# Performance work log

Hardware: AMD Instinct MI355X
Metric: run time of the kernel (lower is better)

The kernel has to match this reference:

```python
import jax, jax.numpy as jnp
import numpy as np

DIM = 512
HEADS = 8
HEAD_DIM = DIM // HEADS
SCALE = HEAD_DIM ** -0.5
CPB_HIDDEN = 512
N_CLASSES = 2
LN_EPS = 1e-5


def _layernorm(x, g, b):
    m = jnp.mean(x, axis=-1, keepdims=True)
    v = jnp.var(x, axis=-1, keepdims=True)
    return (x - m) / jnp.sqrt(v + LN_EPS) * g + b


def _coord_attention(x, coords, cpb_w1, cpb_b1, cpb_w2, cpb_b2, qkv_w, qkv_b, proj_w, proj_b):
    B, N, C = x.shape
    qkv = (x @ qkv_w + qkv_b).reshape(B, N, 3, HEADS, HEAD_DIM)
    q, k, v = jnp.moveaxis(qkv, 2, 0)  # each (B, N, H, hd)
    attn = jnp.einsum('bnhd,bmhd->bhnm', q * SCALE, k)  # (B, H, N, N)
    rel = coords[:, :, None, :] - coords[:, None, :, :]  # (B, N, N, 2)
    rel = rel / (jnp.linalg.norm(rel, axis=-1, keepdims=True) + 1e-6)
    bias = jax.nn.relu(rel @ cpb_w1 + cpb_b1) @ cpb_w2 + cpb_b2  # (B, N, N, H)
    attn = jax.nn.softmax(attn + jnp.transpose(bias, (0, 3, 1, 2)), axis=-1)
    out = jnp.einsum('bhnm,bmhd->bnhd', attn, v).reshape(B, N, C)
    return out @ proj_w + proj_b


def setup_inputs() -> dict:
    key = jax.random.key(0)
    ks = iter(jax.random.split(key, 32))
    d = {}
    d['h'] = jax.random.normal(next(ks), (1, 400, 1024), dtype=jnp.float32)
    d['coords'] = jax.random.uniform(next(ks), (1, 400, 2), dtype=jnp.float32) * 1000.0
    def lin(kw, kb, fan_in, fan_out):
        w = jax.random.normal(kw, (fan_in, fan_out), dtype=jnp.float32) / np.sqrt(fan_in)
        b = jax.random.normal(kb, (fan_out,), dtype=jnp.float32) * 0.01
        return w, b
    d['fc1_w'], d['fc1_b'] = lin(next(ks), next(ks), 1024, DIM)
    d['cls_token'] = jax.random.normal(next(ks), (1, 1, DIM), dtype=jnp.float32)
    for p in ('l1', 'l2'):
        d[p + '_norm_g'] = jnp.ones((DIM,), jnp.float32)
        d[p + '_norm_b'] = jnp.zeros((DIM,), jnp.float32)
        d[p + '_cpb_w1'], d[p + '_cpb_b1'] = lin(next(ks), next(ks), 2, CPB_HIDDEN)
        d[p + '_cpb_w2'], d[p + '_cpb_b2'] = lin(next(ks), next(ks), CPB_HIDDEN, HEADS)
        d[p + '_qkv_w'], d[p + '_qkv_b'] = lin(next(ks), next(ks), DIM, 3 * DIM)
        d[p + '_proj_w'], d[p + '_proj_b'] = lin(next(ks), next(ks), DIM, DIM)
    d['norm_g'] = jnp.ones((DIM,), jnp.float32)
    d['norm_b'] = jnp.zeros((DIM,), jnp.float32)
    d['fc2_w'], d['fc2_b'] = lin(next(ks), next(ks), DIM, N_CLASSES)
    return d


def reference(h, coords, fc1_w, fc1_b, cls_token,
              l1_norm_g, l1_norm_b, l1_cpb_w1, l1_cpb_b1, l1_cpb_w2, l1_cpb_b2,
              l1_qkv_w, l1_qkv_b, l1_proj_w, l1_proj_b,
              l2_norm_g, l2_norm_b, l2_cpb_w1, l2_cpb_b1, l2_cpb_w2, l2_cpb_b2,
              l2_qkv_w, l2_qkv_b, l2_proj_w, l2_proj_b,
              norm_g, norm_b, fc2_w, fc2_b):
    B, Np, _ = h.shape
    h = jax.nn.relu(h @ fc1_w + fc1_b)  # (B, N, 512)
    side = int(np.ceil(np.sqrt(Np)))
    add = side * side - Np  # pad bag to a perfect square (wrap-around copy)
    h = jnp.concatenate([h, h[:, :add, :]], axis=1)
    coords = jnp.concatenate([coords, coords[:, :add, :]], axis=1)
    cls = jnp.broadcast_to(cls_token, (B, 1, DIM))
    h = jnp.concatenate([cls, h], axis=1)
    coords = jnp.concatenate([jnp.zeros((B, 1, 2), h.dtype), coords], axis=1)
    h = h + _coord_attention(_layernorm(h, l1_norm_g, l1_norm_b), coords,
                             l1_cpb_w1, l1_cpb_b1, l1_cpb_w2, l1_cpb_b2,
                             l1_qkv_w, l1_qkv_b, l1_proj_w, l1_proj_b)
    h = h + _coord_attention(_layernorm(h, l2_norm_g, l2_norm_b), coords,
                             l2_cpb_w1, l2_cpb_b1, l2_cpb_w2, l2_cpb_b2,
                             l2_qkv_w, l2_qkv_b, l2_proj_w, l2_proj_b)
    h = _layernorm(h, norm_g, norm_b)[:, 0]  # CLS token
    return h @ fc2_w + fc2_b  # (B, n_classes)
```

## Files before the change

### kernel.cpp

```cpp
#include <hip/hip_runtime.h>
#include <math.h>

#define NP 401
#define DIM 512
#define HEADS 8
#define HD 64
#define LN_EPS 1e-5f
#define ATT_SCALE 0.125f
#define SP 448
#define PLANE (NP * SP)
#define CPB_M 16384
#define TSTRIDE (CPB_M + 64)
#define PS (401L * 1536)

template<bool TB, typename LA, typename LB>
__device__ __forceinline__ void gemm64(
    int kBeg, int kEnd, int tid,
    float (*as)[68], float (*bs)[68], float (&acc)[4][4],
    LA&& loadA, LB&& loadB)
{
    float aR[4], bR[4];
    loadA(kBeg, aR);
    loadB(kBeg, bR);
    for (int k0 = kBeg; k0 < kEnd; k0 += 16) {
        const int arow = tid >> 2, aq = tid & 3;
        as[aq * 4 + 0][arow] = aR[0];
        as[aq * 4 + 1][arow] = aR[1];
        as[aq * 4 + 2][arow] = aR[2];
        as[aq * 4 + 3][arow] = aR[3];
        if (!TB) {
            *(float4*)&bs[tid >> 4][(tid & 15) * 4] =
                make_float4(bR[0], bR[1], bR[2], bR[3]);
        } else {
            bs[aq * 4 + 0][arow] = bR[0];
            bs[aq * 4 + 1][arow] = bR[1];
            bs[aq * 4 + 2][arow] = bR[2];
            bs[aq * 4 + 3][arow] = bR[3];
        }
        __syncthreads();
        float nA[4] = {0.f,0.f,0.f,0.f}, nB[4] = {0.f,0.f,0.f,0.f};
        if (k0 + 16 < kEnd) { loadA(k0 + 16, nA); loadB(k0 + 16, nB); }
        const int tx = tid & 15, ty = tid >> 4;
        #pragma unroll
        for (int kk = 0; kk < 16; ++kk) {
            float4 a4 = *(const float4*)&as[kk][ty * 4];
            float4 b4 = *(const float4*)&bs[kk][tx * 4];
            float av[4] = {a4.x, a4.y, a4.z, a4.w};
            float bv[4] = {b4.x, b4.y, b4.z, b4.w};
            #pragma unroll
            for (int r = 0; r < 4; ++r)
                #pragma unroll
                for (int c = 0; c < 4; ++c)
                    acc[r][c] = fmaf(av[r], bv[c], acc[r][c]);
        }
        __syncthreads();
        #pragma unroll
        for (int j = 0; j < 4; ++j) { aR[j] = nA[j]; bR[j] = nB[j]; }
    }
}

__global__ __launch_bounds__(256) void gemm_split_kernel(
    const float* __restrict__ A, int lda,
    const float* __restrict__ B, int ldb,
    float* __restrict__ P, int ldc, long slice,
    int M, int N, int K, int skN)
{
    __shared__ float as[16][68], bs[16][68];
    const int tid = threadIdx.x;
    const int m0 = blockIdx.x * 64, n0 = blockIdx.y * 64;
    const int sk = blockIdx.z;
    const int KS = ((K + skN * 16 - 1) / (skN * 16)) * 16;
    const int kBeg = sk * KS;
    const int kEnd = (kBeg + KS < K) ? kBeg + KS : K;
    float acc[4][4] = {};

    auto loadA = [&](int k0, float r[4]) {
        r[0] = r[1] = r[2] = r[3] = 0.f;
        int gm = m0 + (tid >> 2);
        if (gm >= M) return;
        int gk = k0 + (tid & 3) * 4;
        const float* p = A + (long)gm * lda + gk;
        if (gk + 3 < kEnd) {
            float4 v = *(const float4*)p;
            r[0] = v.x; r[1] = v.y; r[2] = v.z; r[3] = v.w;
        } else {
            #pragma unroll
            for (int j = 0; j < 4; ++j) if (gk + j < kEnd) r[j] = p[j];
        }
    };
    auto loadB = [&](int k0, float r[4]) {
        r[0] = r[1] = r[2] = r[3] = 0.f;
        int gk = k0 + (tid >> 4);
        if (gk >= kEnd) return;
        int gn = n0 + (tid & 15) * 4;
        const float* p = B + (long)gk * ldb + gn;
        if (gn + 3 < N) {
            float4 v = *(const float4*)p;
            r[0] = v.x; r[1] = v.y; r[2] = v.z; r[3] = v.w;
        } else {
            #pragma unroll
            for (int j = 0; j < 4; ++j) if (gn + j < N) r[j] = p[j];
        }
    };
    if (kBeg < kEnd)
        gemm64<false>(kBeg, kEnd, tid, as, bs, acc, loadA, loadB);

    float* C = P + (long)sk * slice;
    const int tx = tid & 15, ty = tid >> 4;
    #pragma unroll
    for (int r = 0; r < 4; ++r) {
        int m = m0 + ty * 4 + r;
        if (m >= M) continue;
        int n = n0 + tx * 4;
        if (n + 3 < N) {
            *(float4*)&C[(long)m * ldc + n] =
                make_float4(acc[r][0], acc[r][1], acc[r][2], acc[r][3]);
        } else {
            #pragma unroll
            for (int c = 0; c < 4; ++c)
                if (n + c < N) C[(long)m * ldc + n + c] = acc[r][c];
        }
    }
}

__global__ __launch_bounds__(256) void qk_kernel(
    const float* __restrict__ Pq, const float* __restrict__ qkv_b,
    const int* __restrict__ pm, const float* __restrict__ pf,
    const float* __restrict__ T,
    float* __restrict__ S)
{
    __shared__ float as[16][68], bs[16][68];
    const int tid = threadIdx.x;
    const int m0 = blockIdx.x * 64, n0 = blockIdx.y * 64, h = blockIdx.z;
    float acc[4][4] = {};

    auto loadQ = [&](int k0, float r[4]) {
        int gm = m0 + (tid >> 2);
        if (gm > 400) { r[0]=r[1]=r[2]=r[3]=0.f; return; }
        int gk = k0 + (tid & 3) * 4;
        long off = (long)gm * 1536 + h * 64 + gk;
        float4 x = *(const float4*)(Pq + off);
        float4 y = *(const float4*)(Pq + PS + off);
        float4 b = *(const float4*)(qkv_b + h * 64 + gk);
        r[0] = x.x + y.x + b.x; r[1] = x.y + y.y + b.y;
        r[2] = x.z + y.z + b.z; r[3] = x.w + y.w + b.w;
    };
    auto loadK = [&](int k0, float r[4]) {
        int gn = n0 + (tid >> 2);
        if (gn > 400) { r[0]=r[1]=r[2]=r[3]=0.f; return; }
        int gk = k0 + (tid & 3) * 4;
        long off = (long)gn * 1536 + 512 + h * 64 + gk;
        float4 x = *(const float4*)(Pq + off);
        float4 y = *(const float4*)(Pq + PS + off);
        float4 b = *(const float4*)(qkv_b + 512 + h * 64 + gk);
        r[0] = x.x + y.x + b.x; r[1] = x.y + y.y + b.y;
        r[2] = x.z + y.z + b.z; r[3] = x.w + y.w + b.w;
    };
    gemm64<true>(0, 64, tid, as, bs, acc, loadQ, loadK);

    const int tx = tid & 15, ty = tid >> 4;
    const float* Tt = T + (long)h * TSTRIDE;
    float* Sp = S + (long)h * PLANE;
    #pragma unroll
    for (int r = 0; r < 4; ++r) {
        int i = m0 + ty * 4 + r;
        if (i > 400) continue;
        #pragma unroll
        for (int c = 0; c < 4; ++c) {
            int j = n0 + tx * 4 + c;
            if (j > 400) continue;
            int id = i * 416 + j;
            int mm = pm[id];
            float fr = pf[id];
            float t0 = Tt[mm], t1 = Tt[mm + 1];
            Sp[(long)i * SP + j] =
                fmaf(acc[r][c], ATT_SCALE, fmaf(fr, t1 - t0, t0));
        }
    }
}

__global__ __launch_bounds__(256) void pv_kernel(
    const float* __restrict__ S, const float* __restrict__ Pq,
    const float* __restrict__ qkv_b, float* __restrict__ Pv)
{
    __shared__ float as[16][68], bs[16][68];
    const int tid = threadIdx.x;
    const int m0 = blockIdx.x * 64;
    const int h = blockIdx.z >> 3, sk = blockIdx.z & 7;
    const int kBeg = sk * 64;
    const int kEnd = (kBeg + 64 < NP) ? kBeg + 64 : NP;
    float acc[4][4] = {};

    auto loadA = [&](int k0, float r[4]) {
        r[0] = r[1] = r[2] = r[3] = 0.f;
        int gm = m0 + (tid >> 2);
        if (gm > 400) return;
        int gk = k0 + (tid & 3) * 4;
        const float* p = S + (long)h * PLANE + (long)gm * SP + gk;
        if (gk + 3 < kEnd) {
            float4 v = *(const float4*)p;
            r[0] = v.x; r[1] = v.y; r[2] = v.z; r[3] = v.w;
        } else {
            #pragma unroll
            for (int j = 0; j < 4; ++j) if (gk + j < kEnd) r[j] = p[j];
        }
    };
    auto loadB = [&](int k0, float r[4]) {
        r[0] = r[1] = r[2] = r[3] = 0.f;
        int key = k0 + (tid >> 4);
        if (key >= kEnd) return;
        int d = (tid & 15) * 4;
        long off = (long)key * 1536 + 1024 + h * 64 + d;
        float4 x = *(const float4*)(Pq + off);
        float4 y = *(const float4*)(Pq + PS + off);
        float4 b = *(const float4*)(qkv_b + 1024 + h * 64 + d);
        r[0] = x.x + y.x + b.x; r[1] = x.y + y.y + b.y;
        r[2] = x.z + y.z + b.z; r[3] = x.w + y.w + b.w;
    };
    if (kBeg < kEnd)
        gemm64<false>(kBeg, kEnd, tid, as, bs, acc, loadA, loadB);

    float* C = Pv + (long)sk * (401L * 512);
    const int tx = tid & 15, ty = tid >> 4;
    #pragma unroll
    for (int r = 0; r < 4; ++r) {
        int m = m0 + ty * 4 + r;
        if (m > 400) continue;
        *(float4*)&C[(long)m * 512 + h * 64 + tx * 4] =
            make_float4(acc[r][0], acc[r][1], acc[r][2], acc[r][3]);
    }
}

__global__ __launch_bounds__(256) void att_reduce_kernel(
    const float* __restrict__ Pv, float* __restrict__ att)
{
    int idx = (blockIdx.x * 256 + threadIdx.x) * 4;
    if (idx >= 401 * 512) return;
    float4 s = *(const float4*)(Pv + idx);
    #pragma unroll
    for (int k = 1; k < 8; ++k) {
        float4 p = *(const float4*)(Pv + (long)k * 401 * 512 + idx);
        s.x += p.x; s.y += p.y; s.z += p.z; s.w += p.w;
    }
    *(float4*)(att + idx) = s;
}

__global__ __launch_bounds__(256) void softmax_kernel(float* __restrict__ S)
{
    long base = (long)blockIdx.y * PLANE + (long)blockIdx.x * SP;
    int t = threadIdx.x;
    float v0 = (t < NP) ? S[base + t] : -INFINITY;
    float v1 = (t + 256 < NP) ? S[base + t + 256] : -INFINITY;
    float m = fmaxf(v0, v1);
    #pragma unroll
    for (int off = 32; off > 0; off >>= 1) m = fmaxf(m, __shfl_down(m, off));
    __shared__ float pm_[4], psum[4];
    int w = t >> 6, lane = t & 63;
    if (lane == 0) pm_[w] = m;
    __syncthreads();
    float M4 = fmaxf(fmaxf(pm_[0], pm_[1]), fmaxf(pm_[2], pm_[3]));
    float e0 = (t < NP) ? __expf(v0 - M4) : 0.f;
    float e1 = (t + 256 < NP) ? __expf(v1 - M4) : 0.f;
    float s = e0 + e1;
    #pragma unroll
    for (int off = 32; off > 0; off >>= 1) s += __shfl_down(s, off);
    if (lane == 0) psum[w] = s;
    __syncthreads();
    float inv = 1.f / (psum[0] + psum[1] + psum[2] + psum[3]);
    if (t < NP)       S[base + t] = e0 * inv;
    if (t + 256 < NP) S[base + t + 256] = e1 * inv;
}

__global__ __launch_bounds__(256) void rowfuse_kernel(
    const float* __restrict__ P, long slice, int skN, int rowOff,
    const float* __restrict__ bias, int doRelu,
    const float* __restrict__ resid, const float* __restrict__ cls,
    float* __restrict__ h0,
    const float* __restrict__ g, const float* __restrict__ b,
    float* __restrict__ xln,
    const float* __restrict__ fc2w, const float* __restrict__ fc2b,
    float* __restrict__ out)
{
    const int r = blockIdx.x, t = threadIdx.x;
    float v0, v1;
    if (cls && r == 0) {
        v0 = cls[t]; v1 = cls[t + 256];
    } else {
        const float* p = P + (long)(r - rowOff) * DIM;
        v0 = bias[t]; v1 = bias[t + 256];
        for (int k = 0; k < skN; ++k) {
            v0 += p[(long)k * slice + t];
            v1 += p[(long)k * slice + t + 256];
        }
        if (resid) {
            v0 += resid[(long)r * DIM + t];
            v1 += resid[(long)r * DIM + t + 256];
        }
        if (doRelu) { v0 = fmaxf(v0, 0.f); v1 = fmaxf(v1, 0.f); }
    }
    h0[(long)r * DIM + t] = v0;
    h0[(long)r * DIM + t + 256] = v1;
    if (out && r != 0) return;

    float s = v0 + v1, sq = v0 * v0 + v1 * v1;
    #pragma unroll
    for (int off = 32; off > 0; off >>= 1) {
        s += __shfl_down(s, off);
        sq += __shfl_down(sq, off);
    }
    __shared__ float ps[4], pq[4], pc0[4], pc1[4];
    int w = t >> 6, lane = t & 63;
    if (lane == 0) { ps[w] = s; pq[w] = sq; }
    __syncthreads();
    float Sm = ps[0] + ps[1] + ps[2] + ps[3];
    float Q = pq[0] + pq[1] + pq[2] + pq[3];
    float mean = Sm * (1.f / DIM);
    float var = Q * (1.f / DIM) - mean * mean;
    float inv = rsqrtf(var + LN_EPS);
    float n0 = (v0 - mean) * inv * g[t] + b[t];
    float n1 = (v1 - mean) * inv * g[t + 256] + b[t + 256];
    if (!out) {
        xln[(long)r * DIM + t] = n0;
        xln[(long)r * DIM + t + 256] = n1;
    } else {
        float c0 = n0 * fc2w[t * 2]     + n1 * fc2w[(t + 256) * 2];
        float c1 = n0 * fc2w[t * 2 + 1] + n1 * fc2w[(t + 256) * 2 + 1];
        #pragma unroll
        for (int off = 32; off > 0; off >>= 1) {
            c0 += __shfl_down(c0, off);
            c1 += __shfl_down(c1, off);
        }
        if (lane == 0) { pc0[w] = c0; pc1[w] = c1; }
        __syncthreads();
        if (t == 0) {
            out[0] = pc0[0] + pc0[1] + pc0[2] + pc0[3] + fc2b[0];
            out[1] = pc1[0] + pc1[1] + pc1[2] + pc1[3] + fc2b[1];
        }
    }
}

__global__ __launch_bounds__(256) void mega_kernel(
    const float* __restrict__ hin, const float* __restrict__ fc1_w,
    const float* __restrict__ w1_0, const float* __restrict__ b1_0,
    const float* __restrict__ w2_0, const float* __restrict__ b2_0,
    const float* __restrict__ w1_1, const float* __restrict__ b1_1,
    const float* __restrict__ w2_1, const float* __restrict__ b2_1,
    const float* __restrict__ coords,
    float* __restrict__ Pp, float* __restrict__ T,
    int* __restrict__ pm, float* __restrict__ pf)
{
    __shared__ float as[16][68], bs[16][68];
    __shared__ float red[4][64][8];
    const int bid = blockIdx.x, tid = threadIdx.x;

    if (bid < 448) {
        int sk = bid / 56, rem = bid % 56;
        int m0 = (rem % 7) * 64, n0 = (rem / 7) * 64;
        int kBeg = sk * 128, kEnd = kBeg + 128;
        float acc[4][4] = {};
        auto loadA = [&](int k0, float r[4]) {
            r[0]=r[1]=r[2]=r[3]=0.f;
            int gm = m0 + (tid >> 2);
            if (gm >= 400) return;
            int gk = k0 + (tid & 3) * 4;
            float4 v = *(const float4*)(hin + (long)gm * 1024 + gk);
            r[0]=v.x; r[1]=v.y; r[2]=v.z; r[3]=v.w;
        };
        auto loadB = [&](int k0, float r[4]) {
            int gk = k0 + (tid >> 4);
            int gn = n0 + (tid & 15) * 4;
            float4 v = *(const float4*)(fc1_w + (long)gk * 512 + gn);
            r[0]=v.x; r[1]=v.y; r[2]=v.z; r[3]=v.w;
        };
        gemm64<false>(kBeg, kEnd, tid, as, bs, acc, loadA, loadB);
        float* C = Pp + (long)sk * (400L * 512);
        const int tx = tid & 15, ty = tid >> 4;
        #pragma unroll
        for (int r = 0; r < 4; ++r) {
            int m = m0 + ty * 4 + r;
            if (m >= 400) continue;
            *(float4*)&C[(long)m * 512 + n0 + tx * 4] =
                make_float4(acc[r][0], acc[r][1], acc[r][2], acc[r][3]);
        }
    } else if (bid < 962) {
        int tb = bid - 448;
        int z = tb / 257, ab = tb % 257;
        const float* w1 = z ? w1_1 : w1_0;
        const float* b1 = z ? b1_1 : b1_0;
        const float* w2 = z ? w2_1 : w2_0;
        const float* b2 = z ? b2_1 : b2_0;
        const int lane = tid & 63, wv = tid >> 6;
        float ca = 0.f, sa = 0.f;
        if (ab != 256) {
            float th = fmaf((float)(ab * 64 + lane),
                            (float)(2.0 * M_PI / CPB_M), -(float)M_PI);
            sincosf(th, &sa, &ca);
        } else if (lane == 0) {
            sincosf((float)M_PI, &sa, &ca);
        }
        float a8[8] = {};
        const int kbeg = wv * 128;
        #pragma unroll 4
        for (int k = kbeg; k < kbeg + 128; ++k) {
            float hk = fmaxf(fmaf(ca, w1[k], fmaf(sa, w1[512 + k], b1[k])), 0.f);
            #pragma unroll
            for (int h2 = 0; h2 < 8; ++h2)
                a8[h2] = fmaf(hk, w2[k * 8 + h2], a8[h2]);
        }
        #pragma unroll
        for (int h2 = 0; h2 < 8; ++h2) red[wv][lane][h2] = a8[h2];
        __syncthreads();
        if (tid < 64) {
            int a = ab * 64 + tid;
            #pragma unroll
            for (int h2 = 0; h2 < 8; ++h2)
                T[(long)(z * 8 + h2) * TSTRIDE + a] =
                    red[0][tid][h2] + red[1][tid][h2] +
                    red[2][tid][h2] + red[3][tid][h2] + b2[h2];
        }
    } else {
        int p = (bid - 962) * 256 + tid;
        if (p < NP * NP) {
            int i = p / NP, j = p - i * NP;
            float xi = (i == 0) ? 0.f : coords[(i - 1) * 2];
            float yi = (i == 0) ? 0.f : coords[(i - 1) * 2 + 1];
            float xj = (j == 0) ? 0.f : coords[(j - 1) * 2];
            float yj = (j == 0) ? 0.f : coords[(j - 1) * 2 + 1];
            float rx = xi - xj, ry = yi - yj;
            int mm; float fr;
            if (rx == 0.f && ry == 0.f) {
                mm = CPB_M + 1; fr = 0.f;
            } else {
                float x = (atan2f(ry, rx) + 3.14159265358979f)
                          * (float)(CPB_M / (2.0 * M_PI));
                int mi = (int)x;
                fr = x - (float)mi;
                mm = (mi >= CPB_M) ? mi - CPB_M : mi;
            }
            pm[i * 416 + j] = mm;
            pf[i * 416 + j] = fr;
        }
    }
}

extern "C" void kernel_launch(void* const* d_in, const int* in_sizes, int n_in,
                              void* d_out, int out_size, void* d_ws, size_t ws_size,
                              hipStream_t stream)
{
    const float* h      = (const float*)d_in[0];
    const float* coords = (const float*)d_in[1];
    const float* fc1_w  = (const float*)d_in[2];
    const float* fc1_b  = (const float*)d_in[3];
    const float* cls    = (const float*)d_in[4];
    const float* norm_g = (const float*)d_in[25];
    const float* norm_b = (const float*)d_in[26];
    const float* fc2_w  = (const float*)d_in[27];
    const float* fc2_b  = (const float*)d_in[28];

    float* ws  = (float*)d_ws;
    float* h0  = ws;
    float* xln = h0  + 401L * 512;
    float* att = xln + 401L * 512;
    float* S   = att + 401L * 512;
    float* T   = S   + 8L * PLANE;
    int*   pm  = (int*)(T + 16L * TSTRIDE);
    float* pf  = (float*)(pm + 401L * 416);
    float* Pq  = pf + 401L * 416;
    float* Pv  = Pq + 2L * 401 * 1536;
    float* Pp  = Pv + 8L * 401 * 512;

    mega_kernel<<<1591, 256, 0, stream>>>(
        h, fc1_w,
        (const float*)d_in[7],  (const float*)d_in[8],
        (const float*)d_in[9],  (const float*)d_in[10],
        (const float*)d_in[17], (const float*)d_in[18],
        (const float*)d_in[19], (const float*)d_in[20],
        coords, Pp, T, pm, pf);

    rowfuse_kernel<<<401, 256, 0, stream>>>(
        Pp, 400L * 512, 8, 1, fc1_b, 1, nullptr, cls, h0,
        (const float*)d_in[5], (const float*)d_in[6], xln,
        nullptr, nullptr, nullptr);

    for (int l = 0; l < 2; ++l) {
        int base = 5 + 10 * l;
        const float* qkv_w  = (const float*)d_in[base + 6];
        const float* qkv_b  = (const float*)d_in[base + 7];
        const float* proj_w = (const float*)d_in[base + 8];
        const float* proj_b = (const float*)d_in[base + 9];

        gemm_split_kernel<<<dim3(7, 24, 2), 256, 0, stream>>>(
            xln, 512, qkv_w, 1536, Pq, 1536, 401L * 1536, 401, 1536, 512, 2);

        qk_kernel<<<dim3(7, 7, 8), 256, 0, stream>>>(
            Pq, qkv_b, pm, pf, T + (long)l * 8 * TSTRIDE, S);

        softmax_kernel<<<dim3(401, 8), 256, 0, stream>>>(S);

        pv_kernel<<<dim3(7, 1, 64), 256, 0, stream>>>(S, Pq, qkv_b, Pv);
        att_reduce_kernel<<<201, 256, 0, stream>>>(Pv, att);

        gemm_split_kernel<<<dim3(7, 8, 8), 256, 0, stream>>>(
            att, 512, proj_w, 512, Pp, 512, 401L * 512, 401, 512, 512, 8);

        if (l == 0) {
            rowfuse_kernel<<<401, 256, 0, stream>>>(
                Pp, 401L * 512, 8, 0, proj_b, 0, h0, nullptr, h0,
                (const float*)d_in[15], (const float*)d_in[16], xln,
                nullptr, nullptr, nullptr);
        } else {
            rowfuse_kernel<<<401, 256, 0, stream>>>(
                Pp, 401L * 512, 8, 0, proj_b, 0, h0, nullptr, h0,
                norm_g, norm_b, nullptr, fc2_w, fc2_b, (float*)d_out);
        }
    }
}
```

Baseline: 282.2 us.

## Fuse whole forward pass into one persistent kernel with software grid barriers

Replaces the sequence of about fifteen kernel launches with a single persistent kernel of 448 blocks. Each former kernel becomes a phase that blocks walk through with a grid-stride loop, and phases are separated by an atomic-counter grid barrier. The goal is to remove launch overhead and inter-kernel gaps, which matter a lot for this small workload. It also changes split-K factors (for example PV split into two slices of 208) and folds the attention reduction into the projection loads. The cost is that correctness depends on all 448 blocks being co-resident, there is spin-wait overhead at each barrier, and occupancy is limited by the two-blocks-per-SM launch bound.

```diff
diff --git a/kernel.cpp b/kernel.cpp
--- a/kernel.cpp
+++ b/kernel.cpp
@@ -3,8 +3,6 @@
 
 #define NP 401
 #define DIM 512
-#define HEADS 8
-#define HD 64
 #define LN_EPS 1e-5f
 #define ATT_SCALE 0.125f
 #define SP 448
@@ -12,6 +10,46 @@
 #define CPB_M 16384
 #define TSTRIDE (CPB_M + 64)
 #define PS (401L * 1536)
+#define GRID 448
+
+struct KArgs {
+    const float *hin, *coords, *fc1_w, *fc1_b, *cls;
+    const float *l1_ng, *l1_nb, *l1_w1, *l1_b1, *l1_w2, *l1_b2;
+    const float *l1_qkvw, *l1_qkvb, *l1_projw, *l1_projb;
+    const float *l2_ng, *l2_nb, *l2_w1, *l2_b1, *l2_w2, *l2_b2;
+    const float *l2_qkvw, *l2_qkvb, *l2_projw, *l2_projb;
+    const float *norm_g, *norm_b, *fc2_w, *fc2_b;
+    float *h0, *xln, *S, *T;
+    int *pm;
+    float *pf, *Pq, *Pv, *Pp, *out;
+};
+
+__device__ unsigned g_cnt = 0;
+__device__ unsigned g_gen = 0;
+
+__device__ __forceinline__ void gridbar()
+{
+    __syncthreads();
+    if (threadIdx.x == 0) {
+        unsigned g = __hip_atomic_load(&g_gen, __ATOMIC_RELAXED,
+                                       __HIP_MEMORY_SCOPE_AGENT);
+        unsigned old = __hip_atomic_fetch_add(&g_cnt, 1, __ATOMIC_ACQ_REL,
+                                              __HIP_MEMORY_SCOPE_AGENT);
+        if (old == gridDim.x - 1) {
+            __hip_atomic_store(&g_cnt, 0u, __ATOMIC_RELAXED,
+                               __HIP_MEMORY_SCOPE_AGENT);
+            __hip_atomic_fetch_add(&g_gen, 1, __ATOMIC_ACQ_REL,
+                                   __HIP_MEMORY_SCOPE_AGENT);
+        } else {
+            while (__hip_atomic_load(&g_gen, __ATOMIC_RELAXED,
+                                     __HIP_MEMORY_SCOPE_AGENT) == g)
+                __builtin_amdgcn_s_sleep(2);
+            (void)__hip_atomic_load(&g_gen, __ATOMIC_ACQUIRE,
+                                    __HIP_MEMORY_SCOPE_AGENT);
+        }
+    }
+    __syncthreads();
+}
 
 template<bool TB, typename LA, typename LB>
 __device__ __forceinline__ void gemm64(
@@ -59,229 +97,17 @@
     }
 }
 
-__global__ __launch_bounds__(256) void gemm_split_kernel(
-    const float* __restrict__ A, int lda,
-    const float* __restrict__ B, int ldb,
-    float* __restrict__ P, int ldc, long slice,
-    int M, int N, int K, int skN)
-{
-    __shared__ float as[16][68], bs[16][68];
-    const int tid = threadIdx.x;
-    const int m0 = blockIdx.x * 64, n0 = blockIdx.y * 64;
-    const int sk = blockIdx.z;
-    const int KS = ((K + skN * 16 - 1) / (skN * 16)) * 16;
-    const int kBeg = sk * KS;
-    const int kEnd = (kBeg + KS < K) ? kBeg + KS : K;
-    float acc[4][4] = {};
-
-    auto loadA = [&](int k0, float r[4]) {
-        r[0] = r[1] = r[2] = r[3] = 0.f;
-        int gm = m0 + (tid >> 2);
-        if (gm >= M) return;
-        int gk = k0 + (tid & 3) * 4;
-        const float* p = A + (long)gm * lda + gk;
-        if (gk + 3 < kEnd) {
-            float4 v = *(const float4*)p;
-            r[0] = v.x; r[1] = v.y; r[2] = v.z; r[3] = v.w;
-        } else {
-            #pragma unroll
-            for (int j = 0; j < 4; ++j) if (gk + j < kEnd) r[j] = p[j];
-        }
-    };
-    auto loadB = [&](int k0, float r[4]) {
-        r[0] = r[1] = r[2] = r[3] = 0.f;
-        int gk = k0 + (tid >> 4);
-        if (gk >= kEnd) return;
-        int gn = n0 + (tid & 15) * 4;
-        const float* p = B + (long)gk * ldb + gn;
-        if (gn + 3 < N) {
-            float4 v = *(const float4*)p;
-            r[0] = v.x; r[1] = v.y; r[2] = v.z; r[3] = v.w;
-        } else {
-            #pragma unroll
-            for (int j = 0; j < 4; ++j) if (gn + j < N) r[j] = p[j];
-        }
-    };
-    if (kBeg < kEnd)
-        gemm64<false>(kBeg, kEnd, tid, as, bs, acc, loadA, loadB);
-
-    float* C = P + (long)sk * slice;
-    const int tx = tid & 15, ty = tid >> 4;
-    #pragma unroll
-    for (int r = 0; r < 4; ++r) {
-        int m = m0 + ty * 4 + r;
-        if (m >= M) continue;
-        int n = n0 + tx * 4;
-        if (n + 3 < N) {
-            *(float4*)&C[(long)m * ldc + n] =
-                make_float4(acc[r][0], acc[r][1], acc[r][2], acc[r][3]);
-        } else {
-            #pragma unroll
-            for (int c = 0; c < 4; ++c)
-                if (n + c < N) C[(long)m * ldc + n + c] = acc[r][c];
-        }
-    }
-}
-
-__global__ __launch_bounds__(256) void qk_kernel(
-    const float* __restrict__ Pq, const float* __restrict__ qkv_b,
-    const int* __restrict__ pm, const float* __restrict__ pf,
-    const float* __restrict__ T,
-    float* __restrict__ S)
-{
-    __shared__ float as[16][68], bs[16][68];
-    const int tid = threadIdx.x;
-    const int m0 = blockIdx.x * 64, n0 = blockIdx.y * 64, h = blockIdx.z;
-    float acc[4][4] = {};
-
-    auto loadQ = [&](int k0, float r[4]) {
-        int gm = m0 + (tid >> 2);
-        if (gm > 400) { r[0]=r[1]=r[2]=r[3]=0.f; return; }
-        int gk = k0 + (tid & 3) * 4;
-        long off = (long)gm * 1536 + h * 64 + gk;
-        float4 x = *(const float4*)(Pq + off);
-        float4 y = *(const float4*)(Pq + PS + off);
-        float4 b = *(const float4*)(qkv_b + h * 64 + gk);
-        r[0] = x.x + y.x + b.x; r[1] = x.y + y.y + b.y;
-        r[2] = x.z + y.z + b.z; r[3] = x.w + y.w + b.w;
-    };
-    auto loadK = [&](int k0, float r[4]) {
-        int gn = n0 + (tid >> 2);
-        if (gn > 400) { r[0]=r[1]=r[2]=r[3]=0.f; return; }
-        int gk = k0 + (tid & 3) * 4;
-        long off = (long)gn * 1536 + 512 + h * 64 + gk;
-        float4 x = *(const float4*)(Pq + off);
-        float4 y = *(const float4*)(Pq + PS + off);
-        float4 b = *(const float4*)(qkv_b + 512 + h * 64 + gk);
-        r[0] = x.x + y.x + b.x; r[1] = x.y + y.y + b.y;
-        r[2] = x.z + y.z + b.z; r[3] = x.w + y.w + b.w;
-    };
-    gemm64<true>(0, 64, tid, as, bs, acc, loadQ, loadK);
-
-    const int tx = tid & 15, ty = tid >> 4;
-    const float* Tt = T + (long)h * TSTRIDE;
-    float* Sp = S + (long)h * PLANE;
-    #pragma unroll
-    for (int r = 0; r < 4; ++r) {
-        int i = m0 + ty * 4 + r;
-        if (i > 400) continue;
-        #pragma unroll
-        for (int c = 0; c < 4; ++c) {
-            int j = n0 + tx * 4 + c;
-            if (j > 400) continue;
-            int id = i * 416 + j;
-            int mm = pm[id];
-            float fr = pf[id];
-            float t0 = Tt[mm], t1 = Tt[mm + 1];
-            Sp[(long)i * SP + j] =
-                fmaf(acc[r][c], ATT_SCALE, fmaf(fr, t1 - t0, t0));
-        }
-    }
-}
-
-__global__ __launch_bounds__(256) void pv_kernel(
-    const float* __restrict__ S, const float* __restrict__ Pq,
-    const float* __restrict__ qkv_b, float* __restrict__ Pv)
-{
-    __shared__ float as[16][68], bs[16][68];
-    const int tid = threadIdx.x;
-    const int m0 = blockIdx.x * 64;
-    const int h = blockIdx.z >> 3, sk = blockIdx.z & 7;
-    const int kBeg = sk * 64;
-    const int kEnd = (kBeg + 64 < NP) ? kBeg + 64 : NP;
-    float acc[4][4] = {};
-
-    auto loadA = [&](int k0, float r[4]) {
-        r[0] = r[1] = r[2] = r[3] = 0.f;
-        int gm = m0 + (tid >> 2);
-        if (gm > 400) return;
-        int gk = k0 + (tid & 3) * 4;
-        const float* p = S + (long)h * PLANE + (long)gm * SP + gk;
-        if (gk + 3 < kEnd) {
-            float4 v = *(const float4*)p;
-            r[0] = v.x; r[1] = v.y; r[2] = v.z; r[3] = v.w;
-        } else {
-            #pragma unroll
-            for (int j = 0; j < 4; ++j) if (gk + j < kEnd) r[j] = p[j];
-        }
-    };
-    auto loadB = [&](int k0, float r[4]) {
-        r[0] = r[1] = r[2] = r[3] = 0.f;
-        int key = k0 + (tid >> 4);
-        if (key >= kEnd) return;
-        int d = (tid & 15) * 4;
-        long off = (long)key * 1536 + 1024 + h * 64 + d;
-        float4 x = *(const float4*)(Pq + off);
-        float4 y = *(const float4*)(Pq + PS + off);
-        float4 b = *(const float4*)(qkv_b + 1024 + h * 64 + d);
-        r[0] = x.x + y.x + b.x; r[1] = x.y + y.y + b.y;
-        r[2] = x.z + y.z + b.z; r[3] = x.w + y.w + b.w;
-    };
-    if (kBeg < kEnd)
-        gemm64<false>(kBeg, kEnd, tid, as, bs, acc, loadA, loadB);
-
-    float* C = Pv + (long)sk * (401L * 512);
-    const int tx = tid & 15, ty = tid >> 4;
-    #pragma unroll
-    for (int r = 0; r < 4; ++r) {
-        int m = m0 + ty * 4 + r;
-        if (m > 400) continue;
-        *(float4*)&C[(long)m * 512 + h * 64 + tx * 4] =
-            make_float4(acc[r][0], acc[r][1], acc[r][2], acc[r][3]);
-    }
-}
-
-__global__ __launch_bounds__(256) void att_reduce_kernel(
-    const float* __restrict__ Pv, float* __restrict__ att)
-{
-    int idx = (blockIdx.x * 256 + threadIdx.x) * 4;
-    if (idx >= 401 * 512) return;
-    float4 s = *(const float4*)(Pv + idx);
-    #pragma unroll
-    for (int k = 1; k < 8; ++k) {
-        float4 p = *(const float4*)(Pv + (long)k * 401 * 512 + idx);
-        s.x += p.x; s.y += p.y; s.z += p.z; s.w += p.w;
-    }
-    *(float4*)(att + idx) = s;
-}
-
-__global__ __launch_bounds__(256) void softmax_kernel(float* __restrict__ S)
-{
-    long base = (long)blockIdx.y * PLANE + (long)blockIdx.x * SP;
-    int t = threadIdx.x;
-    float v0 = (t < NP) ? S[base + t] : -INFINITY;
-    float v1 = (t + 256 < NP) ? S[base + t + 256] : -INFINITY;
-    float m = fmaxf(v0, v1);
-    #pragma unroll
-    for (int off = 32; off > 0; off >>= 1) m = fmaxf(m, __shfl_down(m, off));
-    __shared__ float pm_[4], psum[4];
-    int w = t >> 6, lane = t & 63;
-    if (lane == 0) pm_[w] = m;
-    __syncthreads();
-    float M4 = fmaxf(fmaxf(pm_[0], pm_[1]), fmaxf(pm_[2], pm_[3]));
-    float e0 = (t < NP) ? __expf(v0 - M4) : 0.f;
-    float e1 = (t + 256 < NP) ? __expf(v1 - M4) : 0.f;
-    float s = e0 + e1;
-    #pragma unroll
-    for (int off = 32; off > 0; off >>= 1) s += __shfl_down(s, off);
-    if (lane == 0) psum[w] = s;
-    __syncthreads();
-    float inv = 1.f / (psum[0] + psum[1] + psum[2] + psum[3]);
-    if (t < NP)       S[base + t] = e0 * inv;
-    if (t + 256 < NP) S[base + t + 256] = e1 * inv;
-}
-
-__global__ __launch_bounds__(256) void rowfuse_kernel(
-    const float* __restrict__ P, long slice, int skN, int rowOff,
+__device__ void rowfuse_unit(
+    int r, const float* __restrict__ P, long slice, int skN, int rowOff,
     const float* __restrict__ bias, int doRelu,
     const float* __restrict__ resid, const float* __restrict__ cls,
     float* __restrict__ h0,
     const float* __restrict__ g, const float* __restrict__ b,
     float* __restrict__ xln,
     const float* __restrict__ fc2w, const float* __restrict__ fc2b,
-    float* __restrict__ out)
+    float* __restrict__ out, float* __restrict__ sm)
 {
-    const int r = blockIdx.x, t = threadIdx.x;
+    const int t = threadIdx.x;
     float v0, v1;
     if (cls && r == 0) {
         v0 = cls[t]; v1 = cls[t + 256];
@@ -308,12 +134,11 @@
         s += __shfl_down(s, off);
         sq += __shfl_down(sq, off);
     }
-    __shared__ float ps[4], pq[4], pc0[4], pc1[4];
     int w = t >> 6, lane = t & 63;
-    if (lane == 0) { ps[w] = s; pq[w] = sq; }
+    if (lane == 0) { sm[w] = s; sm[4 + w] = sq; }
     __syncthreads();
-    float Sm = ps[0] + ps[1] + ps[2] + ps[3];
-    float Q = pq[0] + pq[1] + pq[2] + pq[3];
+    float Sm = sm[0] + sm[1] + sm[2] + sm[3];
+    float Q = sm[4] + sm[5] + sm[6] + sm[7];
     float mean = Sm * (1.f / DIM);
     float var = Q * (1.f / DIM) - mean * mean;
     float inv = rsqrtf(var + LN_EPS);
@@ -322,6 +147,7 @@
     if (!out) {
         xln[(long)r * DIM + t] = n0;
         xln[(long)r * DIM + t + 256] = n1;
+        __syncthreads();
     } else {
         float c0 = n0 * fc2w[t * 2]     + n1 * fc2w[(t + 256) * 2];
         float c1 = n0 * fc2w[t * 2 + 1] + n1 * fc2w[(t + 256) * 2 + 1];
@@ -330,115 +156,333 @@
             c0 += __shfl_down(c0, off);
             c1 += __shfl_down(c1, off);
         }
-        if (lane == 0) { pc0[w] = c0; pc1[w] = c1; }
+        if (lane == 0) { sm[8 + w] = c0; sm[12 + w] = c1; }
         __syncthreads();
         if (t == 0) {
-            out[0] = pc0[0] + pc0[1] + pc0[2] + pc0[3] + fc2b[0];
-            out[1] = pc1[0] + pc1[1] + pc1[2] + pc1[3] + fc2b[1];
+            out[0] = sm[8] + sm[9] + sm[10] + sm[11] + fc2b[0];
+            out[1] = sm[12] + sm[13] + sm[14] + sm[15] + fc2b[1];
         }
     }
 }
 
-__global__ __launch_bounds__(256) void mega_kernel(
-    const float* __restrict__ hin, const float* __restrict__ fc1_w,
-    const float* __restrict__ w1_0, const float* __restrict__ b1_0,
-    const float* __restrict__ w2_0, const float* __restrict__ b2_0,
-    const float* __restrict__ w1_1, const float* __restrict__ b1_1,
-    const float* __restrict__ w2_1, const float* __restrict__ b2_1,
-    const float* __restrict__ coords,
-    float* __restrict__ Pp, float* __restrict__ T,
-    int* __restrict__ pm, float* __restrict__ pf)
+__global__ __launch_bounds__(256, 2) void persist_kernel(KArgs a)
 {
-    __shared__ float as[16][68], bs[16][68];
-    __shared__ float red[4][64][8];
+    __shared__ float smem[2176];
+    float (*as)[68] = (float(*)[68])smem;
+    float (*bs)[68] = (float(*)[68])(smem + 1088);
+    float (*red)[64][8] = (float(*)[64][8])smem;
     const int bid = blockIdx.x, tid = threadIdx.x;
-
-    if (bid < 448) {
-        int sk = bid / 56, rem = bid % 56;
-        int m0 = (rem % 7) * 64, n0 = (rem / 7) * 64;
-        int kBeg = sk * 128, kEnd = kBeg + 128;
-        float acc[4][4] = {};
-        auto loadA = [&](int k0, float r[4]) {
-            r[0]=r[1]=r[2]=r[3]=0.f;
-            int gm = m0 + (tid >> 2);
-            if (gm >= 400) return;
-            int gk = k0 + (tid & 3) * 4;
-            float4 v = *(const float4*)(hin + (long)gm * 1024 + gk);
-            r[0]=v.x; r[1]=v.y; r[2]=v.z; r[3]=v.w;
-        };
-        auto loadB = [&](int k0, float r[4]) {
-            int gk = k0 + (tid >> 4);
-            int gn = n0 + (tid & 15) * 4;
-            float4 v = *(const float4*)(fc1_w + (long)gk * 512 + gn);
-            r[0]=v.x; r[1]=v.y; r[2]=v.z; r[3]=v.w;
-        };
-        gemm64<false>(kBeg, kEnd, tid, as, bs, acc, loadA, loadB);
-        float* C = Pp + (long)sk * (400L * 512);
-        const int tx = tid & 15, ty = tid >> 4;
-        #pragma unroll
-        for (int r = 0; r < 4; ++r) {
-            int m = m0 + ty * 4 + r;
-            if (m >= 400) continue;
-            *(float4*)&C[(long)m * 512 + n0 + tx * 4] =
-                make_float4(acc[r][0], acc[r][1], acc[r][2], acc[r][3]);
-        }
-    } else if (bid < 962) {
-        int tb = bid - 448;
-        int z = tb / 257, ab = tb % 257;
-        const float* w1 = z ? w1_1 : w1_0;
-        const float* b1 = z ? b1_1 : b1_0;
-        const float* w2 = z ? w2_1 : w2_0;
-        const float* b2 = z ? b2_1 : b2_0;
-        const int lane = tid & 63, wv = tid >> 6;
-        float ca = 0.f, sa = 0.f;
-        if (ab != 256) {
-            float th = fmaf((float)(ab * 64 + lane),
-                            (float)(2.0 * M_PI / CPB_M), -(float)M_PI);
-            sincosf(th, &sa, &ca);
-        } else if (lane == 0) {
-            sincosf((float)M_PI, &sa, &ca);
-        }
-        float a8[8] = {};
-        const int kbeg = wv * 128;
-        #pragma unroll 4
-        for (int k = kbeg; k < kbeg + 128; ++k) {
-            float hk = fmaxf(fmaf(ca, w1[k], fmaf(sa, w1[512 + k], b1[k])), 0.f);
-            #pragma unroll
-            for (int h2 = 0; h2 < 8; ++h2)
-                a8[h2] = fmaf(hk, w2[k * 8 + h2], a8[h2]);
-        }
-        #pragma unroll
-        for (int h2 = 0; h2 < 8; ++h2) red[wv][lane][h2] = a8[h2];
-        __syncthreads();
-        if (tid < 64) {
-            int a = ab * 64 + tid;
-            #pragma unroll
-            for (int h2 = 0; h2 < 8; ++h2)
-                T[(long)(z * 8 + h2) * TSTRIDE + a] =
-                    red[0][tid][h2] + red[1][tid][h2] +
-                    red[2][tid][h2] + red[3][tid][h2] + b2[h2];
-        }
-    } else {
-        int p = (bid - 962) * 256 + tid;
-        if (p < NP * NP) {
-            int i = p / NP, j = p - i * NP;
-            float xi = (i == 0) ? 0.f : coords[(i - 1) * 2];
-            float yi = (i == 0) ? 0.f : coords[(i - 1) * 2 + 1];
-            float xj = (j == 0) ? 0.f : coords[(j - 1) * 2];
-            float yj = (j == 0) ? 0.f : coords[(j - 1) * 2 + 1];
-            float rx = xi - xj, ry = yi - yj;
-            int mm; float fr;
-            if (rx == 0.f && ry == 0.f) {
-                mm = CPB_M + 1; fr = 0.f;
-            } else {
-                float x = (atan2f(ry, rx) + 3.14159265358979f)
-                          * (float)(CPB_M / (2.0 * M_PI));
-                int mi = (int)x;
-                fr = x - (float)mi;
-                mm = (mi >= CPB_M) ? mi - CPB_M : mi;
-            }
-            pm[i * 416 + j] = mm;
-            pf[i * 416 + j] = fr;
+    const int tx = tid & 15, ty = tid >> 4;
+
+    for (int u = bid; u < 1591; u += GRID) {
+        if (u < 448) {
+            int sk = u / 56, rem = u % 56;
+            int m0 = (rem % 7) * 64, n0 = (rem / 7) * 64;
+            int kBeg = sk * 128, kEnd = kBeg + 128;
+            float acc[4][4] = {};
+            auto loadA = [&](int k0, float r[4]) {
+                r[0]=r[1]=r[2]=r[3]=0.f;
+                int gm = m0 + (tid >> 2);
+                if (gm >= 400) return;
+                int gk = k0 + (tid & 3) * 4;
+                float4 v = *(const float4*)(a.hin + (long)gm * 1024 + gk);
+                r[0]=v.x; r[1]=v.y; r[2]=v.z; r[3]=v.w;
+            };
+            auto loadB = [&](int k0, float r[4]) {
+                int gk = k0 + (tid >> 4);
+                int gn = n0 + (tid & 15) * 4;
+                float4 v = *(const float4*)(a.fc1_w + (long)gk * 512 + gn);
+                r[0]=v.x; r[1]=v.y; r[2]=v.z; r[3]=v.w;
+            };
+            gemm64<false>(kBeg, kEnd, tid, as, bs, acc, loadA, loadB);
+            float* C = a.Pp + (long)sk * (400L * 512);
+            #pragma unroll
+            for (int r = 0; r < 4; ++r) {
+                int m = m0 + ty * 4 + r;
+                if (m >= 400) continue;
+                *(float4*)&C[(long)m * 512 + n0 + tx * 4] =
+                    make_float4(acc[r][0], acc[r][1], acc[r][2], acc[r][3]);
+            }
+        } else if (u < 962) {
+            int tb = u - 448;
+            int z = tb / 257, ab = tb % 257;
+            const float* w1 = z ? a.l2_w1 : a.l1_w1;
+            const float* b1 = z ? a.l2_b1 : a.l1_b1;
+            const float* w2 = z ? a.l2_w2 : a.l1_w2;
+            const float* b2 = z ? a.l2_b2 : a.l1_b2;
+            const int lane = tid & 63, wv = tid >> 6;
+            float ca = 0.f, sa = 0.f;
+            if (ab != 256) {
+                float th = fmaf((float)(ab * 64 + lane),
+                                (float)(2.0 * M_PI / CPB_M), -(float)M_PI);
+                sincosf(th, &sa, &ca);
+            } else if (lane == 0) {
+                sincosf((float)M_PI, &sa, &ca);
+            }
+            float a8[8] = {};
+            const int kbeg = wv * 128;
+            #pragma unroll 4
+            for (int k = kbeg; k < kbeg + 128; ++k) {
+                float hk = fmaxf(fmaf(ca, w1[k],
+                                      fmaf(sa, w1[512 + k], b1[k])), 0.f);
+                #pragma unroll
+                for (int h2 = 0; h2 < 8; ++h2)
+                    a8[h2] = fmaf(hk, w2[k * 8 + h2], a8[h2]);
+            }
+            #pragma unroll
+            for (int h2 = 0; h2 < 8; ++h2) red[wv][lane][h2] = a8[h2];
+            __syncthreads();
+            if (tid < 64) {
+                int aidx = ab * 64 + tid;
+                #pragma unroll
+                for (int h2 = 0; h2 < 8; ++h2)
+                    a.T[(long)(z * 8 + h2) * TSTRIDE + aidx] =
+                        red[0][tid][h2] + red[1][tid][h2] +
+                        red[2][tid][h2] + red[3][tid][h2] + b2[h2];
+            }
+            __syncthreads();
+        } else {
+            int p = (u - 962) * 256 + tid;
+            if (p < NP * NP) {
+                int i = p / NP, j = p - i * NP;
+                float xi = (i == 0) ? 0.f : a.coords[(i - 1) * 2];
+                float yi = (i == 0) ? 0.f : a.coords[(i - 1) * 2 + 1];
+                float xj = (j == 0) ? 0.f : a.coords[(j - 1) * 2];
+                float yj = (j == 0) ? 0.f : a.coords[(j - 1) * 2 + 1];
+                float rx = xi - xj, ry = yi - yj;
+                int mm; float fr;
+                if (rx == 0.f && ry == 0.f) {
+                    mm = CPB_M + 1; fr = 0.f;
+                } else {
+                    float x = (atan2f(ry, rx) + 3.14159265358979f)
+                              * (float)(CPB_M / (2.0 * M_PI));
+                    int mi = (int)x;
+                    fr = x - (float)mi;
+                    mm = (mi >= CPB_M) ? mi - CPB_M : mi;
+                }
+                a.pm[i * 416 + j] = mm;
+                a.pf[i * 416 + j] = fr;
+            }
+        }
+    }
+    gridbar();
+
+    for (int u = bid; u < 401; u += GRID)
+        rowfuse_unit(u, a.Pp, 400L * 512, 8, 1, a.fc1_b, 1, nullptr, a.cls,
+                     a.h0, a.l1_ng, a.l1_nb, a.xln,
+                     nullptr, nullptr, nullptr, smem);
+    gridbar();
+
+    for (int l = 0; l < 2; ++l) {
+        const float* qkvw  = l ? a.l2_qkvw  : a.l1_qkvw;
+        const float* qkvb  = l ? a.l2_qkvb  : a.l1_qkvb;
+        const float* projw = l ? a.l2_projw : a.l1_projw;
+        const float* projb = l ? a.l2_projb : a.l1_projb;
+        const float* Tl = a.T + (long)l * 8 * TSTRIDE;
+
+        for (int u = bid; u < 336; u += GRID) {
+            int sk = u / 168, rem = u % 168;
+            int m0 = (rem % 7) * 64, n0 = (rem / 7) * 64;
+            int kBeg = sk * 256, kEnd = kBeg + 256;
+            float acc[4][4] = {};
+            auto loadA = [&](int k0, float r[4]) {
+                r[0]=r[1]=r[2]=r[3]=0.f;
+                int gm = m0 + (tid >> 2);
+                if (gm > 400) return;
+                int gk = k0 + (tid & 3) * 4;
+                float4 v = *(const float4*)(a.xln + (long)gm * 512 + gk);
+                r[0]=v.x; r[1]=v.y; r[2]=v.z; r[3]=v.w;
+            };
+            auto loadB = [&](int k0, float r[4]) {
+                int gk = k0 + (tid >> 4);
+                int gn = n0 + (tid & 15) * 4;
+                float4 v = *(const float4*)(qkvw + (long)gk * 1536 + gn);
+                r[0]=v.x; r[1]=v.y; r[2]=v.z; r[3]=v.w;
+            };
+            gemm64<false>(kBeg, kEnd, tid, as, bs, acc, loadA, loadB);
+            float* C = a.Pq + (long)sk * PS;
+            #pragma unroll
+            for (int r = 0; r < 4; ++r) {
+                int m = m0 + ty * 4 + r;
+                if (m > 400) continue;
+                *(float4*)&C[(long)m * 1536 + n0 + tx * 4] =
+                    make_float4(acc[r][0], acc[r][1], acc[r][2], acc[r][3]);
+            }
+        }
+        gridbar();
+
+        for (int u = bid; u < 392; u += GRID) {
+            int h = u / 49, rem = u % 49;
+            int m0 = (rem % 7) * 64, n0 = (rem / 7) * 64;
+            float acc[4][4] = {};
+            auto loadQ = [&](int k0, float r[4]) {
+                int gm = m0 + (tid >> 2);
+                if (gm > 400) { r[0]=r[1]=r[2]=r[3]=0.f; return; }
+                int gk = k0 + (tid & 3) * 4;
+                long off = (long)gm * 1536 + h * 64 + gk;
+                float4 x = *(const float4*)(a.Pq + off);
+                float4 y = *(const float4*)(a.Pq + PS + off);
+                float4 b = *(const float4*)(qkvb + h * 64 + gk);
+                r[0] = x.x + y.x + b.x; r[1] = x.y + y.y + b.y;
+                r[2] = x.z + y.z + b.z; r[3] = x.w + y.w + b.w;
+            };
+            auto loadK = [&](int k0, float r[4]) {
+                int gn = n0 + (tid >> 2);
+                if (gn > 400) { r[0]=r[1]=r[2]=r[3]=0.f; return; }
+                int gk = k0 + (tid & 3) * 4;
+                long off = (long)gn * 1536 + 512 + h * 64 + gk;
+                float4 x = *(const float4*)(a.Pq + off);
+                float4 y = *(const float4*)(a.Pq + PS + off);
+                float4 b = *(const float4*)(qkvb + 512 + h * 64 + gk);
+                r[0] = x.x + y.x + b.x; r[1] = x.y + y.y + b.y;
+                r[2] = x.z + y.z + b.z; r[3] = x.w + y.w + b.w;
+            };
+            gemm64<true>(0, 64, tid, as, bs, acc, loadQ, loadK);
+            const float* Tt = Tl + (long)h * TSTRIDE;
+            float* Sp = a.S + (long)h * PLANE;
+            #pragma unroll
+            for (int r = 0; r < 4; ++r) {
+                int i = m0 + ty * 4 + r;
+                if (i > 400) continue;
+                #pragma unroll
+                for (int c = 0; c < 4; ++c) {
+                    int j = n0 + tx * 4 + c;
+                    if (j > 400) continue;
+                    int id = i * 416 + j;
+                    int mm = a.pm[id];
+                    float fr = a.pf[id];
+                    float t0 = Tt[mm], t1 = Tt[mm + 1];
+                    Sp[(long)i * SP + j] =
+                        fmaf(acc[r][c], ATT_SCALE, fmaf(fr, t1 - t0, t0));
+                }
+            }
+        }
+        gridbar();
+
+        for (int u = bid; u < 802; u += GRID) {
+            int r = u * 4 + (tid >> 6);
+            if (r < 3208) {
+                int hh = r / 401, i = r - hh * 401;
+                float* row = a.S + (long)hh * PLANE + (long)i * SP;
+                int lane = tid & 63;
+                float v[7], mx = -INFINITY;
+                #pragma unroll
+                for (int j = 0; j < 7; ++j) {
+                    int c = lane + j * 64;
+                    v[j] = (c < NP) ? row[c] : -INFINITY;
+                    mx = fmaxf(mx, v[j]);
+                }
+                #pragma unroll
+                for (int off = 32; off > 0; off >>= 1)
+                    mx = fmaxf(mx, __shfl_xor(mx, off));
+                float s = 0.f;
+                #pragma unroll
+                for (int j = 0; j < 7; ++j) {
+                    v[j] = (lane + j * 64 < NP) ? __expf(v[j] - mx) : 0.f;
+                    s += v[j];
+                }
+                #pragma unroll
+                for (int off = 32; off > 0; off >>= 1)
+                    s += __shfl_xor(s, off);
+                float inv = 1.f / s;
+                #pragma unroll
+                for (int j = 0; j < 7; ++j) {
+                    int c = lane + j * 64;
+                    if (c < NP) row[c] = v[j] * inv;
+                }
+            }
+        }
+        gridbar();
+
+        for (int u = bid; u < 112; u += GRID) {
+            int sk = u / 56, rem = u % 56;
+            int m0 = (rem % 7) * 64, h = rem / 7;
+            int kBeg = sk * 208;
+            int kEnd = (kBeg + 208 < NP) ? kBeg + 208 : NP;
+            float acc[4][4] = {};
+            auto loadA = [&](int k0, float r[4]) {
+                r[0]=r[1]=r[2]=r[3]=0.f;
+                int gm = m0 + (tid >> 2);
+                if (gm > 400) return;
+                int gk = k0 + (tid & 3) * 4;
+                const float* p = a.S + (long)h * PLANE + (long)gm * SP + gk;
+                if (gk + 3 < kEnd) {
+                    float4 v = *(const float4*)p;
+                    r[0]=v.x; r[1]=v.y; r[2]=v.z; r[3]=v.w;
+                } else {
+                    #pragma unroll
+                    for (int j = 0; j < 4; ++j) if (gk + j < kEnd) r[j] = p[j];
+                }
+            };
+            auto loadB = [&](int k0, float r[4]) {
+                r[0]=r[1]=r[2]=r[3]=0.f;
+                int key = k0 + (tid >> 4);
+                if (key >= kEnd) return;
+                int d = (tid & 15) * 4;
+                long off = (long)key * 1536 + 1024 + h * 64 + d;
+                float4 x = *(const float4*)(a.Pq + off);
+                float4 y = *(const float4*)(a.Pq + PS + off);
+                float4 b = *(const float4*)(qkvb + 1024 + h * 64 + d);
+                r[0] = x.x + y.x + b.x; r[1] = x.y + y.y + b.y;
+                r[2] = x.z + y.z + b.z; r[3] = x.w + y.w + b.w;
+            };
+            gemm64<false>(kBeg, kEnd, tid, as, bs, acc, loadA, loadB);
+            float* C = a.Pv + (long)sk * (401L * 512);
+            #pragma unroll
+            for (int r = 0; r < 4; ++r) {
+                int m = m0 + ty * 4 + r;
+                if (m > 400) continue;
+                *(float4*)&C[(long)m * 512 + h * 64 + tx * 4] =
+                    make_float4(acc[r][0], acc[r][1], acc[r][2], acc[r][3]);
+            }
+        }
+        gridbar();
+
+        for (int u = bid; u < 448; u += GRID) {
+            int sk = u / 56, rem = u % 56;
+            int m0 = (rem % 7) * 64, n0 = (rem / 7) * 64;
+            int kBeg = sk * 64, kEnd = kBeg + 64;
+            float acc[4][4] = {};
+            auto loadA = [&](int k0, float r[4]) {
+                r[0]=r[1]=r[2]=r[3]=0.f;
+                int gm = m0 + (tid >> 2);
+                if (gm > 400) return;
+                int gk = k0 + (tid & 3) * 4;
+                long off = (long)gm * 512 + gk;
+                float4 x = *(const float4*)(a.Pv + off);
+                float4 y = *(const float4*)(a.Pv + 401L * 512 + off);
+                r[0] = x.x + y.x; r[1] = x.y + y.y;
+                r[2] = x.z + y.z; r[3] = x.w + y.w;
+            };
+            auto loadB = [&](int k0, float r[4]) {
+                int gk = k0 + (tid >> 4);
+                int gn = n0 + (tid & 15) * 4;
+                float4 v = *(const float4*)(projw + (long)gk * 512 + gn);
+                r[0]=v.x; r[1]=v.y; r[2]=v.z; r[3]=v.w;
+            };
+            gemm64<false>(kBeg, kEnd, tid, as, bs, acc, loadA, loadB);
+            float* C = a.Pp + (long)sk * (401L * 512);
+            #pragma unroll
+            for (int r = 0; r < 4; ++r) {
+                int m = m0 + ty * 4 + r;
+                if (m > 400) continue;
+                *(float4*)&C[(long)m * 512 + n0 + tx * 4] =
+                    make_float4(acc[r][0], acc[r][1], acc[r][2], acc[r][3]);
+            }
+        }
+        gridbar();
+
+        if (l == 0) {
+            for (int u = bid; u < 401; u += GRID)
+                rowfuse_unit(u, a.Pp, 401L * 512, 8, 0, projb, 0, a.h0,
+                             nullptr, a.h0, a.l2_ng, a.l2_nb, a.xln,
+                             nullptr, nullptr, nullptr, smem);
+            gridbar();
+        } else {
+            if (bid == 0)
+                rowfuse_unit(0, a.Pp, 401L * 512, 8, 0, projb, 0, a.h0,
+                             nullptr, a.h0, a.norm_g, a.norm_b, nullptr,
+                             a.fc2_w, a.fc2_b, a.out, smem);
         }
     }
 }
@@ -447,71 +491,36 @@
                               void* d_out, int out_size, void* d_ws, size_t ws_size,
                               hipStream_t stream)
 {
-    const float* h      = (const float*)d_in[0];
-    const float* coords = (const float*)d_in[1];
-    const float* fc1_w  = (const float*)d_in[2];
-    const float* fc1_b  = (const float*)d_in[3];
-    const float* cls    = (const float*)d_in[4];
-    const float* norm_g = (const float*)d_in[25];
-    const float* norm_b = (const float*)d_in[26];
-    const float* fc2_w  = (const float*)d_in[27];
-    const float* fc2_b  = (const float*)d_in[28];
-
     float* ws  = (float*)d_ws;
-    float* h0  = ws;
-    float* xln = h0  + 401L * 512;
-    float* att = xln + 401L * 512;
-    float* S   = att + 401L * 512;
-    float* T   = S   + 8L * PLANE;
-    int*   pm  = (int*)(T + 16L * TSTRIDE);
-    float* pf  = (float*)(pm + 401L * 416);
-    float* Pq  = pf + 401L * 416;
-    float* Pv  = Pq + 2L * 401 * 1536;
-    float* Pp  = Pv + 8L * 401 * 512;
-
-    mega_kernel<<<1591, 256, 0, stream>>>(
-        h, fc1_w,
-        (const float*)d_in[7],  (const float*)d_in[8],
-        (const float*)d_in[9],  (const float*)d_in[10],
-        (const float*)d_in[17], (const float*)d_in[18],
-        (const float*)d_in[19], (const float*)d_in[20],
-        coords, Pp, T, pm, pf);
-
-    rowfuse_kernel<<<401, 256, 0, stream>>>(
-        Pp, 400L * 512, 8, 1, fc1_b, 1, nullptr, cls, h0,
-        (const float*)d_in[5], (const float*)d_in[6], xln,
-        nullptr, nullptr, nullptr);
-
-    for (int l = 0; l < 2; ++l) {
-        int base = 5 + 10 * l;
-        const float* qkv_w  = (const float*)d_in[base + 6];
-        const float* qkv_b  = (const float*)d_in[base + 7];
-        const float* proj_w = (const float*)d_in[base + 8];
-        const float* proj_b = (const float*)d_in[base + 9];
-
-        gemm_split_kernel<<<dim3(7, 24, 2), 256, 0, stream>>>(
-            xln, 512, qkv_w, 1536, Pq, 1536, 401L * 1536, 401, 1536, 512, 2);
-
-        qk_kernel<<<dim3(7, 7, 8), 256, 0, stream>>>(
-            Pq, qkv_b, pm, pf, T + (long)l * 8 * TSTRIDE, S);
-
-        softmax_kernel<<<dim3(401, 8), 256, 0, stream>>>(S);
-
-        pv_kernel<<<dim3(7, 1, 64), 256, 0, stream>>>(S, Pq, qkv_b, Pv);
-        att_reduce_kernel<<<201, 256, 0, stream>>>(Pv, att);
-
-        gemm_split_kernel<<<dim3(7, 8, 8), 256, 0, stream>>>(
-            att, 512, proj_w, 512, Pp, 512, 401L * 512, 401, 512, 512, 8);
-
-        if (l == 0) {
-            rowfuse_kernel<<<401, 256, 0, stream>>>(
-                Pp, 401L * 512, 8, 0, proj_b, 0, h0, nullptr, h0,
-                (const float*)d_in[15], (const float*)d_in[16], xln,
-                nullptr, nullptr, nullptr);
-        } else {
-            rowfuse_kernel<<<401, 256, 0, stream>>>(
-                Pp, 401L * 512, 8, 0, proj_b, 0, h0, nullptr, h0,
-                norm_g, norm_b, nullptr, fc2_w, fc2_b, (float*)d_out);
-        }
-    }
+    KArgs a;
+    a.hin    = (const float*)d_in[0];
+    a.coords = (const float*)d_in[1];
+    a.fc1_w  = (const float*)d_in[2];
+    a.fc1_b  = (const float*)d_in[3];
+    a.cls    = (const float*)d_in[4];
+    a.l1_ng  = (const float*)d_in[5];   a.l1_nb  = (const float*)d_in[6];
+    a.l1_w1  = (const float*)d_in[7];   a.l1_b1  = (const float*)d_in[8];
+    a.l1_w2  = (const float*)d_in[9];   a.l1_b2  = (const float*)d_in[10];
+    a.l1_qkvw = (const float*)d_in[11]; a.l1_qkvb = (const float*)d_in[12];
+    a.l1_projw = (const float*)d_in[13]; a.l1_projb = (const float*)d_in[14];
+    a.l2_ng  = (const float*)d_in[15];  a.l2_nb  = (const float*)d_in[16];
+    a.l2_w1  = (const float*)d_in[17];  a.l2_b1  = (const float*)d_in[18];
+    a.l2_w2  = (const float*)d_in[19];  a.l2_b2  = (const float*)d_in[20];
+    a.l2_qkvw = (const float*)d_in[21]; a.l2_qkvb = (const float*)d_in[22];
+    a.l2_projw = (const float*)d_in[23]; a.l2_projb = (const float*)d_in[24];
+    a.norm_g = (const float*)d_in[25];  a.norm_b = (const float*)d_in[26];
+    a.fc2_w  = (const float*)d_in[27];  a.fc2_b  = (const float*)d_in[28];
+
+    a.h0  = ws;                          ws += 401L * 512;
+    a.xln = ws;                          ws += 401L * 512;
+    a.S   = ws;                          ws += 8L * PLANE;
+    a.T   = ws;                          ws += 16L * TSTRIDE;
+    a.pm  = (int*)ws;                    ws += 401L * 416;
+    a.pf  = ws;                          ws += 401L * 416;
+    a.Pq  = ws;                          ws += 2L * 401 * 1536;
+    a.Pv  = ws;                          ws += 2L * 401 * 512;
+    a.Pp  = ws;                          ws += 8L * 401 * 512;
+    a.out = (float*)d_out;
+
+    persist_kernel<<<GRID, 256, 0, stream>>>(a);
 }
```

Measured after the change: 855.5 us. 3.03x slower.
